# Kernel tuning notes

Hardware: AMD Instinct MI355X
Metric: run time of the kernel (lower is better)

The kernel has to match this reference:

```python
import jax, jax.numpy as jnp
import numpy as np

N, L, D, H, HIST = 4, 1024, 1024, 16, 128
HD = D // H          # head_dim = 64
SCALE = D ** 0.5     # note: original scales by sqrt(model_dim), not sqrt(head_dim)


def _band_mask():
    # get_mask: tril XOR tril(diag=-history_len) -> True inside the causal band.
    # masked_fill fills where mask is True, so pass the complement (True outside band).
    r = jnp.arange(L)[:, None]
    c = jnp.arange(L)[None, :]
    band = (c <= r) & (c > r - HIST)  # band of width HIST incl. diagonal
    return jnp.broadcast_to(~band, (N, 1, L, L))


def setup_inputs() -> dict:
    key = jax.random.key(0)
    ks = jax.random.split(key, 8)
    s = 0.02
    return {
        "values": jax.random.normal(ks[0], (N, L, D), jnp.float32),
        "keys": jax.random.normal(ks[1], (N, L, D), jnp.float32),
        "query": jax.random.normal(ks[2], (N, L, D), jnp.float32),
        "mask": _band_mask(),
        "Wv": jax.random.normal(ks[3], (HD, HD), jnp.float32) * s,
        "Wk": jax.random.normal(ks[4], (HD, HD), jnp.float32) * s,
        "Wq": jax.random.normal(ks[5], (HD, HD), jnp.float32) * s,
        "Wo": jax.random.normal(ks[6], (D, D), jnp.float32) * s,
        "bo": jax.random.normal(ks[7], (D,), jnp.float32) * s,
    }


def reference(values, keys, query, mask, Wv, Wk, Wq, Wo, bo):
    n, qlen, _ = query.shape
    # split heads and apply per-head linear projections (nn.Linear: x @ W.T)
    v = values.reshape(n, -1, H, HD) @ Wv.T
    k = keys.reshape(n, -1, H, HD) @ Wk.T
    q = query.reshape(n, qlen, H, HD) @ Wq.T
    # full energy [n, h, q, k]
    energy = jnp.einsum('nqhd,nkhd->nhqk', q, k)
    energy = jnp.where(mask, jnp.float32(-1e20), energy)
    scores = jax.nn.softmax(energy / SCALE, axis=-1)
    # NOTE: faithful to original einsum 'nhql,nlhd->nlhd' (reduces over q):
    # attention[n,l,h,d] = (sum_q scores[n,h,q,l]) * v[n,l,h,d]
    attention = jnp.einsum('nhql,nlhd->nlhd', scores, v)
    out = attention.reshape(n, qlen, D) @ Wo.T + bo
    return out
```

## Files before the change

kernel.cpp:

```cpp
#include <hip/hip_runtime.h>
#include <hip/hip_bf16.h>
#include <math.h>


using short8 = __attribute__((ext_vector_type(8))) short;
using f32x4  = __attribute__((ext_vector_type(4))) float;

__device__ __forceinline__ unsigned short f2bf(float x) {
    unsigned u = __float_as_uint(x);
    u += 0x7FFFu + ((u >> 16) & 1u);
    return (unsigned short)(u >> 16);
}

__global__ __launch_bounds__(256) void k_stage(const float* __restrict__ keys,
                                               const float* __restrict__ query,
                                               const float* __restrict__ Wq,
                                               const float* __restrict__ Wk,
                                               const float* __restrict__ Wv,
                                               const float4* __restrict__ Wo4,
                                               unsigned short* __restrict__ kk2p,
                                               unsigned short* __restrict__ qb,
                                               ushort4* __restrict__ wob4,
                                               unsigned short* __restrict__ Wvb,
                                               float* __restrict__ w) {
    __shared__ unsigned short Ml[64 * 64];

    const int b = blockIdx.x, tid = threadIdx.x;

    if (b < 1024) {
        const int wv = tid >> 6, lane = tid & 63;
        const int m = lane & 15, q4 = lane >> 4, ksel = q4 * 8;

        {
            short8 aM0, aM1;
#pragma unroll
            for (int j = 0; j < 8; ++j) {
                aM0[j] = (short)f2bf(Wq[(ksel + j) * 64 + wv * 16 + m]);
                aM1[j] = (short)f2bf(Wq[(32 + ksel + j) * 64 + wv * 16 + m]);
            }
#pragma unroll
            for (int fc = 0; fc < 4; ++fc) {
                short8 bM0, bM1;
#pragma unroll
                for (int j = 0; j < 8; ++j) {
                    bM0[j] = (short)f2bf(Wk[(ksel + j) * 64 + fc * 16 + m]);
                    bM1[j] = (short)f2bf(Wk[(32 + ksel + j) * 64 + fc * 16 + m]);
                }
                f32x4 a = f32x4{0.f, 0.f, 0.f, 0.f};
                a = __builtin_amdgcn_mfma_f32_16x16x32_bf16(aM0, bM0, a, 0, 0, 0);
                a = __builtin_amdgcn_mfma_f32_16x16x32_bf16(aM1, bM1, a, 0, 0, 0);
#pragma unroll
                for (int r = 0; r < 4; ++r)
                    Ml[(wv * 16 + q4 * 4 + r) * 64 + fc * 16 + m] =
                        f2bf(a[r] * (1.0f / 32.0f));
            }
        }
        __syncthreads();

        const long R0 = (long)b * 64;
        const float* ka = keys + (R0 + wv * 16 + m) * 64;
        short8 af[2];
#pragma unroll
        for (int ch = 0; ch < 2; ++ch) {
            float4 x0 = *reinterpret_cast<const float4*>(ka + ch * 32 + ksel);
            float4 x1 = *reinterpret_cast<const float4*>(ka + ch * 32 + ksel + 4);
            short8 a;
            a[0] = (short)f2bf(x0.x); a[1] = (short)f2bf(x0.y);
            a[2] = (short)f2bf(x0.z); a[3] = (short)f2bf(x0.w);
            a[4] = (short)f2bf(x1.x); a[5] = (short)f2bf(x1.y);
            a[6] = (short)f2bf(x1.z); a[7] = (short)f2bf(x1.w);
            af[ch] = a;
        }

        f32x4 acc[4];
#pragma unroll
        for (int fc = 0; fc < 4; ++fc) {
            acc[fc] = f32x4{0.f, 0.f, 0.f, 0.f};
#pragma unroll
            for (int ch = 0; ch < 2; ++ch) {
                short8 bf = *reinterpret_cast<const short8*>(
                    &Ml[(fc * 16 + m) * 64 + ch * 32 + ksel]);
                acc[fc] = __builtin_amdgcn_mfma_f32_16x16x32_bf16(af[ch], bf, acc[fc], 0, 0, 0);
            }
        }

        const long rowb = R0 + wv * 16 + (lane >> 4) * 4;
#pragma unroll
        for (int reg = 0; reg < 4; ++reg) {
            long rg = rowb + reg;
            int hh = (int)(rg & 15);
            int ll = (int)((rg >> 4) & 1023);
            int nn = (int)(rg >> 14);
            unsigned short* orow = kk2p + ((size_t)((nn * 16 + hh) * 1024 + ll)) * 64;
#pragma unroll
            for (int fc = 0; fc < 4; ++fc)
                orow[fc * 16 + m] = f2bf(acc[fc][reg]);
        }
    } else if (b < 2048) {
        const int bb = b - 1024;
        const int tile = bb & 15, nh = bb >> 4, h = nh & 15, n = nh >> 4;
        const int t0 = tile * 64;
        const float* qbase = query + ((size_t)(n * 1024 + t0)) * 1024 + h * 64;
        unsigned short* qout = qb + ((size_t)(nh * 1024 + t0)) * 64;
#pragma unroll
        for (int i = 0; i < 4; ++i) {
            int idx = tid + i * 256;
            int r = idx >> 4, f0 = (idx & 15) * 4;
            float4 qv = *reinterpret_cast<const float4*>(qbase + (size_t)r * 1024 + f0);
            ushort4 qo; qo.x = f2bf(qv.x); qo.y = f2bf(qv.y);
            qo.z = f2bf(qv.z); qo.w = f2bf(qv.w);
            *reinterpret_cast<ushort4*>(qout + (size_t)r * 64 + f0) = qo;
        }
    } else if (b < 3072) {
        const int bb = b - 2048;
        int idx = bb * 256 + tid;
        float4 v = Wo4[idx];
        ushort4 o; o.x = f2bf(v.x); o.y = f2bf(v.y);
        o.z = f2bf(v.z); o.w = f2bf(v.w);
        wob4[idx] = o;
        if (bb < 256) w[bb * 256 + tid] = 0.f;
    } else {
        int idx = (b - 3072) * 256 + tid;
        Wvb[idx] = f2bf(Wv[idx]);
    }
}

__global__ __launch_bounds__(256) void k_w2(const unsigned short* __restrict__ qb,
                                            const unsigned short* __restrict__ kk2p,
                                            float* __restrict__ w) {
    __shared__ float wloc[192];

    const int tid  = threadIdx.x;
    const int b    = blockIdx.x;
    const int nh   = b & 63;
    const int tile = b >> 6;
    const int t0   = tile * 64;

    if (tid < 192) wloc[tid] = 0.f;
    __syncthreads();

    const int wv = tid >> 6, lane = tid & 63;
    const int m = lane & 15, q4 = lane >> 4, ksel = q4 * 8;

    const unsigned short* qrow = qb + ((size_t)(nh * 1024 + t0 + wv * 16 + m)) * 64;
    short8 af0 = *reinterpret_cast<const short8*>(qrow + ksel);
    short8 af1 = *reinterpret_cast<const short8*>(qrow + 32 + ksel);

    const unsigned short* kb = kk2p + (size_t)nh * 1024 * 64;

    f32x4 acc[12];
#pragma unroll
    for (int ni = 0; ni < 12; ++ni) {
        int l = t0 - 127 + ni * 16 + m;
        int lc = min(max(l, 0), 1023);
        const unsigned short* kp = kb + (size_t)lc * 64 + ksel;
        short8 b0 = *reinterpret_cast<const short8*>(kp);
        short8 b1 = *reinterpret_cast<const short8*>(kp + 32);
        f32x4 a = f32x4{0.f, 0.f, 0.f, 0.f};
        a = __builtin_amdgcn_mfma_f32_16x16x32_bf16(af0, b0, a, 0, 0, 0);
        a = __builtin_amdgcn_mfma_f32_16x16x32_bf16(af1, b1, a, 0, 0, 0);
        acc[ni] = a;
    }

    const int rbase = wv * 16 + q4 * 4;
    float rs[4] = {0.f, 0.f, 0.f, 0.f};
#pragma unroll
    for (int ni = 0; ni < 12; ++ni) {
        const int c = ni * 16 + m;
#pragma unroll
        for (int reg = 0; reg < 4; ++reg) {
            const int rlw = rbase + reg;
            bool valid = (c >= rlw) && (c <= rlw + 127) && (c + t0 >= 127);
            float e = valid ? __expf(acc[ni][reg]) : 0.f;
            acc[ni][reg] = e;
            rs[reg] += e;
        }
    }
#pragma unroll
    for (int reg = 0; reg < 4; ++reg) {
#pragma unroll
        for (int mm = 1; mm < 16; mm <<= 1) rs[reg] += __shfl_xor(rs[reg], mm);
        rs[reg] = 1.0f / rs[reg];
    }
#pragma unroll
    for (int ni = 0; ni < 12; ++ni) {
        float cs = acc[ni][0] * rs[0] + acc[ni][1] * rs[1] +
                   acc[ni][2] * rs[2] + acc[ni][3] * rs[3];
        cs += __shfl_xor(cs, 16);
        cs += __shfl_xor(cs, 32);
        if (lane < 16) atomicAdd(&wloc[ni * 16 + m], cs);
    }
    __syncthreads();

    for (int c = tid; c < 192; c += 256) {
        int l = t0 - 127 + c;
        if (l >= 0 && l < 1024)
            atomicAdd(&w[(size_t)nh * 1024 + l], wloc[c]);
    }
}

__global__ __launch_bounds__(256) void k_ap2(const float* __restrict__ values,
                                             const unsigned short* __restrict__ Wvb,
                                             const float* __restrict__ w,
                                             unsigned short* __restrict__ apb) {
    const int tid = threadIdx.x;
    const long R0 = (long)blockIdx.x * 64;
    const int wv = tid >> 6, lane = tid & 63;
    const int m = lane & 15, ksel = (lane >> 4) * 8;

    const float* va = values + (R0 + wv * 16 + m) * 64;
    short8 af[2];
#pragma unroll
    for (int ch = 0; ch < 2; ++ch) {
        float4 x0 = *reinterpret_cast<const float4*>(va + ch * 32 + ksel);
        float4 x1 = *reinterpret_cast<const float4*>(va + ch * 32 + ksel + 4);
        short8 a;
        a[0] = (short)f2bf(x0.x); a[1] = (short)f2bf(x0.y);
        a[2] = (short)f2bf(x0.z); a[3] = (short)f2bf(x0.w);
        a[4] = (short)f2bf(x1.x); a[5] = (short)f2bf(x1.y);
        a[6] = (short)f2bf(x1.z); a[7] = (short)f2bf(x1.w);
        af[ch] = a;
    }

    f32x4 acc[4];
#pragma unroll
    for (int dc = 0; dc < 4; ++dc) {
        acc[dc] = f32x4{0.f, 0.f, 0.f, 0.f};
#pragma unroll
        for (int ch = 0; ch < 2; ++ch) {
            short8 bf = *reinterpret_cast<const short8*>(
                Wvb + (size_t)(dc * 16 + m) * 64 + ch * 32 + ksel);
            acc[dc] = __builtin_amdgcn_mfma_f32_16x16x32_bf16(af[ch], bf, acc[dc], 0, 0, 0);
        }
    }

    const long rowb = R0 + wv * 16 + (lane >> 4) * 4;
    float wf[4];
#pragma unroll
    for (int reg = 0; reg < 4; ++reg) {
        long rg = rowb + reg;
        int hh = (int)(rg & 15);
        int ll = (int)((rg >> 4) & 1023);
        int nn = (int)(rg >> 14);
        wf[reg] = w[((size_t)(nn * 16 + hh) << 10) + ll];
    }
#pragma unroll
    for (int dc = 0; dc < 4; ++dc)
#pragma unroll
        for (int reg = 0; reg < 4; ++reg)
            apb[(size_t)(rowb + reg) * 64 + dc * 16 + m] = f2bf(acc[dc][reg] * wf[reg]);
}

__global__ __launch_bounds__(256) void k_out_mfma(
    const unsigned short* __restrict__ apb,
    const unsigned short* __restrict__ wob,
    const float* __restrict__ bo,
    float* __restrict__ out) {
    __shared__ unsigned short As[2][128 * 32];
    __shared__ unsigned short Bs[2][64 * 32];

    const int tid  = threadIdx.x;
    const int wv   = tid >> 6;
    const int lane = tid & 63;
    const int m    = lane & 15;

    const int by = blockIdx.x & 31;
    const int bx = blockIdx.x >> 5;
    const long arow0 = (long)by * 128;
    const int  bcol0 = bx * 64;

    f32x4 acc[2][4];
#pragma unroll
    for (int mi = 0; mi < 2; ++mi)
#pragma unroll
        for (int ni = 0; ni < 4; ++ni) acc[mi][ni] = f32x4{0.f, 0.f, 0.f, 0.f};

    const int r0s = tid >> 2;
    const int kks = (tid & 3) * 8;

    for (int kt = 0; kt < 16; ++kt) {
        const int k0 = kt * 64;
#pragma unroll
        for (int hh = 0; hh < 2; ++hh) {
            const int kh = k0 + hh * 32;
#pragma unroll
            for (int i = 0; i < 2; ++i) {
                const unsigned short* g =
                    apb + (arow0 + i * 64 + r0s) * 1024 + kh + kks;
                __builtin_amdgcn_global_load_lds(
                    (const __attribute__((address_space(1))) unsigned int*)g,
                    (__attribute__((address_space(3))) unsigned int*)&As[hh][i * 2048 + wv * 512],
                    16, 0, 0);
            }
            {
                const unsigned short* g =
                    wob + (size_t)(bcol0 + r0s) * 1024 + kh + kks;
                __builtin_amdgcn_global_load_lds(
                    (const __attribute__((address_space(1))) unsigned int*)g,
                    (__attribute__((address_space(3))) unsigned int*)&Bs[hh][wv * 512],
                    16, 0, 0);
            }
        }
        __syncthreads();

        const int koff = (lane >> 4) * 8;
        const int rA = wv * 32 + m;
        short8 af[2][2], bf[4][2];
#pragma unroll
        for (int hh = 0; hh < 2; ++hh) {
#pragma unroll
            for (int mi = 0; mi < 2; ++mi)
                af[mi][hh] = *reinterpret_cast<const short8*>(
                    &As[hh][(rA + mi * 16) * 32 + koff]);
#pragma unroll
            for (int ni = 0; ni < 4; ++ni)
                bf[ni][hh] = *reinterpret_cast<const short8*>(
                    &Bs[hh][(ni * 16 + m) * 32 + koff]);
        }
#pragma unroll
        for (int mi = 0; mi < 2; ++mi)
#pragma unroll
            for (int ni = 0; ni < 4; ++ni) {
                acc[mi][ni] = __builtin_amdgcn_mfma_f32_16x16x32_bf16(
                    af[mi][0], bf[ni][0], acc[mi][ni], 0, 0, 0);
                acc[mi][ni] = __builtin_amdgcn_mfma_f32_16x16x32_bf16(
                    af[mi][1], bf[ni][1], acc[mi][ni], 0, 0, 0);
            }
        __syncthreads();
    }

    const int colb = bcol0 + m;
    const int rowb = (int)arow0 + wv * 32 + (lane >> 4) * 4;
#pragma unroll
    for (int ni = 0; ni < 4; ++ni) {
        const int col = colb + ni * 16;
        const float bias = bo[col];
#pragma unroll
        for (int mi = 0; mi < 2; ++mi) {
            const int row = rowb + mi * 16;
#pragma unroll
            for (int r = 0; r < 4; ++r)
                out[(size_t)(row + r) * 1024 + col] = acc[mi][ni][r] + bias;
        }
    }
}

extern "C" void kernel_launch(void* const* d_in, const int* in_sizes, int n_in,
                              void* d_out, int out_size, void* d_ws, size_t ws_size,
                              hipStream_t stream) {
    const float* values = (const float*)d_in[0];
    const float* keys   = (const float*)d_in[1];
    const float* query  = (const float*)d_in[2];
    const float* Wv     = (const float*)d_in[4];
    const float* Wk     = (const float*)d_in[5];
    const float* Wq     = (const float*)d_in[6];
    const float* Wo     = (const float*)d_in[7];
    const float* bo     = (const float*)d_in[8];
    float* out = (float*)d_out;

    float* w             = (float*)d_ws;
    unsigned short* Wvb  = (unsigned short*)(w + 65536);
    unsigned short* wob  = Wvb + 4096;
    unsigned short* kk2p = wob + 1024 * 1024;
    unsigned short* qb   = kk2p + 64 * 1024 * 64;
    unsigned short* apb  = qb + 64 * 1024 * 64;

    k_stage<<<3088, 256, 0, stream>>>(keys, query, Wq, Wk, Wv, (const float4*)Wo,
                                      kk2p, qb, (ushort4*)wob, Wvb, w);
    k_w2<<<1024, 256, 0, stream>>>(qb, kk2p, w);
    k_ap2<<<1024, 256, 0, stream>>>(values, Wvb, w, apb);
    k_out_mfma<<<512, 256, 0, stream>>>(apb, wob, bo, out);
}
```

Measured before the change: 157.6 us.

## Fuse query bf16 conversion into k_w2 and double-buffer output GEMM LDS

The query fp32-to-bf16 staging pass in k_stage and its qb workspace buffer are removed. k_w2 now reads query rows in fp32 directly and converts them in registers, which avoids one global write and re-read of the query tensor. Separately, k_out_mfma gains double-buffered LDS tiles so the next K-tile's global_load_lds is issued before computing on the current one, overlapping loads with MFMA. This doubles LDS use in the output GEMM, and k_w2 now does strided fp32 reads.

```diff
diff --git a/kernel.cpp b/kernel.cpp
--- a/kernel.cpp
+++ b/kernel.cpp
@@ -13,13 +13,11 @@
 }
 
 __global__ __launch_bounds__(256) void k_stage(const float* __restrict__ keys,
-                                               const float* __restrict__ query,
                                                const float* __restrict__ Wq,
                                                const float* __restrict__ Wk,
                                                const float* __restrict__ Wv,
                                                const float4* __restrict__ Wo4,
                                                unsigned short* __restrict__ kk2p,
-                                               unsigned short* __restrict__ qb,
                                                ushort4* __restrict__ wob4,
                                                unsigned short* __restrict__ Wvb,
                                                float* __restrict__ w) {
@@ -98,21 +96,6 @@
         }
     } else if (b < 2048) {
         const int bb = b - 1024;
-        const int tile = bb & 15, nh = bb >> 4, h = nh & 15, n = nh >> 4;
-        const int t0 = tile * 64;
-        const float* qbase = query + ((size_t)(n * 1024 + t0)) * 1024 + h * 64;
-        unsigned short* qout = qb + ((size_t)(nh * 1024 + t0)) * 64;
-#pragma unroll
-        for (int i = 0; i < 4; ++i) {
-            int idx = tid + i * 256;
-            int r = idx >> 4, f0 = (idx & 15) * 4;
-            float4 qv = *reinterpret_cast<const float4*>(qbase + (size_t)r * 1024 + f0);
-            ushort4 qo; qo.x = f2bf(qv.x); qo.y = f2bf(qv.y);
-            qo.z = f2bf(qv.z); qo.w = f2bf(qv.w);
-            *reinterpret_cast<ushort4*>(qout + (size_t)r * 64 + f0) = qo;
-        }
-    } else if (b < 3072) {
-        const int bb = b - 2048;
         int idx = bb * 256 + tid;
         float4 v = Wo4[idx];
         ushort4 o; o.x = f2bf(v.x); o.y = f2bf(v.y);
@@ -120,12 +103,12 @@
         wob4[idx] = o;
         if (bb < 256) w[bb * 256 + tid] = 0.f;
     } else {
-        int idx = (b - 3072) * 256 + tid;
+        int idx = (b - 2048) * 256 + tid;
         Wvb[idx] = f2bf(Wv[idx]);
     }
 }
 
-__global__ __launch_bounds__(256) void k_w2(const unsigned short* __restrict__ qb,
+__global__ __launch_bounds__(256) void k_w2(const float* __restrict__ query,
                                             const unsigned short* __restrict__ kk2p,
                                             float* __restrict__ w) {
     __shared__ float wloc[192];
@@ -135,6 +118,7 @@
     const int nh   = b & 63;
     const int tile = b >> 6;
     const int t0   = tile * 64;
+    const int h    = nh & 15, n = nh >> 4;
 
     if (tid < 192) wloc[tid] = 0.f;
     __syncthreads();
@@ -142,9 +126,21 @@
     const int wv = tid >> 6, lane = tid & 63;
     const int m = lane & 15, q4 = lane >> 4, ksel = q4 * 8;
 
-    const unsigned short* qrow = qb + ((size_t)(nh * 1024 + t0 + wv * 16 + m)) * 64;
-    short8 af0 = *reinterpret_cast<const short8*>(qrow + ksel);
-    short8 af1 = *reinterpret_cast<const short8*>(qrow + 32 + ksel);
+    const float* qrow = query +
+        ((size_t)(n * 1024 + t0 + wv * 16 + m)) * 1024 + h * 64;
+    float4 x0 = *reinterpret_cast<const float4*>(qrow + ksel);
+    float4 x1 = *reinterpret_cast<const float4*>(qrow + ksel + 4);
+    float4 x2 = *reinterpret_cast<const float4*>(qrow + 32 + ksel);
+    float4 x3 = *reinterpret_cast<const float4*>(qrow + 32 + ksel + 4);
+    short8 af0, af1;
+    af0[0] = (short)f2bf(x0.x); af0[1] = (short)f2bf(x0.y);
+    af0[2] = (short)f2bf(x0.z); af0[3] = (short)f2bf(x0.w);
+    af0[4] = (short)f2bf(x1.x); af0[5] = (short)f2bf(x1.y);
+    af0[6] = (short)f2bf(x1.z); af0[7] = (short)f2bf(x1.w);
+    af1[0] = (short)f2bf(x2.x); af1[1] = (short)f2bf(x2.y);
+    af1[2] = (short)f2bf(x2.z); af1[3] = (short)f2bf(x2.w);
+    af1[4] = (short)f2bf(x3.x); af1[5] = (short)f2bf(x3.y);
+    af1[6] = (short)f2bf(x3.z); af1[7] = (short)f2bf(x3.w);
 
     const unsigned short* kb = kk2p + (size_t)nh * 1024 * 64;
 
@@ -256,8 +252,8 @@
     const unsigned short* __restrict__ wob,
     const float* __restrict__ bo,
     float* __restrict__ out) {
-    __shared__ unsigned short As[2][128 * 32];
-    __shared__ unsigned short Bs[2][64 * 32];
+    __shared__ unsigned short As[2][2][128 * 32];
+    __shared__ unsigned short Bs[2][2][64 * 32];
 
     const int tid  = threadIdx.x;
     const int wv   = tid >> 6;
@@ -278,7 +274,7 @@
     const int r0s = tid >> 2;
     const int kks = (tid & 3) * 8;
 
-    for (int kt = 0; kt < 16; ++kt) {
+    auto stage = [&](int buf, int kt) {
         const int k0 = kt * 64;
 #pragma unroll
         for (int hh = 0; hh < 2; ++hh) {
@@ -289,7 +285,7 @@
                     apb + (arow0 + i * 64 + r0s) * 1024 + kh + kks;
                 __builtin_amdgcn_global_load_lds(
                     (const __attribute__((address_space(1))) unsigned int*)g,
-                    (__attribute__((address_space(3))) unsigned int*)&As[hh][i * 2048 + wv * 512],
+                    (__attribute__((address_space(3))) unsigned int*)&As[buf][hh][i * 2048 + wv * 512],
                     16, 0, 0);
             }
             {
@@ -297,11 +293,18 @@
                     wob + (size_t)(bcol0 + r0s) * 1024 + kh + kks;
                 __builtin_amdgcn_global_load_lds(
                     (const __attribute__((address_space(1))) unsigned int*)g,
-                    (__attribute__((address_space(3))) unsigned int*)&Bs[hh][wv * 512],
+                    (__attribute__((address_space(3))) unsigned int*)&Bs[buf][hh][wv * 512],
                     16, 0, 0);
             }
         }
-        __syncthreads();
+    };
+
+    stage(0, 0);
+    __syncthreads();
+
+    int cur = 0;
+    for (int kt = 0; kt < 16; ++kt) {
+        if (kt < 15) stage(cur ^ 1, kt + 1);
 
         const int koff = (lane >> 4) * 8;
         const int rA = wv * 32 + m;
@@ -311,11 +314,11 @@
 #pragma unroll
             for (int mi = 0; mi < 2; ++mi)
                 af[mi][hh] = *reinterpret_cast<const short8*>(
-                    &As[hh][(rA + mi * 16) * 32 + koff]);
+                    &As[cur][hh][(rA + mi * 16) * 32 + koff]);
 #pragma unroll
             for (int ni = 0; ni < 4; ++ni)
                 bf[ni][hh] = *reinterpret_cast<const short8*>(
-                    &Bs[hh][(ni * 16 + m) * 32 + koff]);
+                    &Bs[cur][hh][(ni * 16 + m) * 32 + koff]);
         }
 #pragma unroll
         for (int mi = 0; mi < 2; ++mi)
@@ -327,6 +330,7 @@
                     af[mi][1], bf[ni][1], acc[mi][ni], 0, 0, 0);
             }
         __syncthreads();
+        cur ^= 1;
     }
 
     const int colb = bcol0 + m;
@@ -362,12 +366,11 @@
     unsigned short* Wvb  = (unsigned short*)(w + 65536);
     unsigned short* wob  = Wvb + 4096;
     unsigned short* kk2p = wob + 1024 * 1024;
-    unsigned short* qb   = kk2p + 64 * 1024 * 64;
-    unsigned short* apb  = qb + 64 * 1024 * 64;
-
-    k_stage<<<3088, 256, 0, stream>>>(keys, query, Wq, Wk, Wv, (const float4*)Wo,
-                                      kk2p, qb, (ushort4*)wob, Wvb, w);
-    k_w2<<<1024, 256, 0, stream>>>(qb, kk2p, w);
+    unsigned short* apb  = kk2p + 64 * 1024 * 64;
+
+    k_stage<<<2064, 256, 0, stream>>>(keys, Wq, Wk, Wv, (const float4*)Wo,
+                                      kk2p, (ushort4*)wob, Wvb, w);
+    k_w2<<<1024, 256, 0, stream>>>(query, kk2p, w);
     k_ap2<<<1024, 256, 0, stream>>>(values, Wvb, w, apb);
     k_out_mfma<<<512, 256, 0, stream>>>(apb, wob, bo, out);
 }
```

Result: no change. 156.7 us, median of 2 (-0.5%).
